# Kernel optimization log

Measured on AMD Instinct MI355X. Metric: run time of the kernel, lower is better.

Reference implementation:

```python
import jax, jax.numpy as jnp
import numpy as np

N = 100000   # num nodes
D = 128      # node_emb_dim
R = 8        # num_relations
E = 1600000  # num edges


def setup_inputs() -> dict:
    key = jax.random.key(0)
    k0, k1, k2, k3, k4 = jax.random.split(key, 5)
    x = jax.random.normal(k0, (N, D), dtype=jnp.float32)
    edge_index = jax.random.randint(k1, (2, E), 0, N, dtype=jnp.int32)
    edge_type = jax.random.randint(k2, (E,), 0, R, dtype=jnp.int32)
    scale = 1.0 / np.sqrt(D)
    W = (jax.random.normal(k3, (R, D, D), dtype=jnp.float32) * scale)       # per-relation weight
    W_root = (jax.random.normal(k4, (D, D), dtype=jnp.float32) * scale)     # root (self-loop) weight
    bias = jnp.zeros((D,), dtype=jnp.float32)
    return {"x": x, "W": W, "W_root": W_root, "bias": bias,
            "edge_index": edge_index, "edge_type": edge_type}


def reference(x, W, W_root, bias, edge_index, edge_type):
    # PyG RGCNConv (num_bases=None, aggr='mean', root_weight=True, bias=True):
    # out_i = x_i @ W_root + bias + sum_r mean_{j in N_r(i)} x_j @ W_r
    # Mean aggregation is linear, so aggregate neighbor features per (node, relation)
    # first, then apply the per-relation transform (avoids [E,D,D] intermediates).
    src, dst = edge_index[0], edge_index[1]
    seg = dst * R + edge_type                                   # [E] segment id per (dst, rel)
    cnt = jax.ops.segment_sum(jnp.ones((E,), x.dtype), seg, num_segments=N * R)  # [N*R]
    sums = jax.ops.segment_sum(x[src], seg, num_segments=N * R)                   # [N*R, D]
    mean = sums / jnp.maximum(cnt, 1.0)[:, None]                                  # [N*R, D]
    rel_out = jnp.einsum('nrd,rde->ne', mean.reshape(N, R, D), W)                 # [N, D]
    return rel_out + x @ W_root + bias
```

## Files before the change

kernel.cpp:

```cpp
#include <hip/hip_runtime.h>


constexpr int D = 128;
constexpr int R = 8;
constexpr int TILE = 2048;
constexpr int CW = 64;
constexpr int LDA = 40;

typedef __bf16 bf16x8 __attribute__((ext_vector_type(8)));
typedef float  f32x4  __attribute__((ext_vector_type(4)));
typedef unsigned short u16x8 __attribute__((ext_vector_type(8)));
typedef unsigned short u16x4 __attribute__((ext_vector_type(4)));

__device__ __forceinline__ unsigned short f2bf(float f) {
    unsigned u = __builtin_bit_cast(unsigned, f);
    u += 0x7FFFu + ((u >> 16) & 1u);
    return (unsigned short)(u >> 16);
}
__device__ __forceinline__ float bf2f(unsigned short h) {
    return __builtin_bit_cast(float, (unsigned)h << 16);
}

constexpr int XB = 768;
constexpr int CB = 512;
__global__ __launch_bounds__(256)
void pre_kernel(const float* __restrict__ x, unsigned short* __restrict__ xbf, int nquad,
                const int* __restrict__ dst, const int* __restrict__ et,
                int* __restrict__ meta, int E) {
    if (blockIdx.x < XB) {
        int stride = XB * 256;
        for (int i = blockIdx.x * 256 + threadIdx.x; i < nquad; i += stride) {
            float4 v = ((const float4*)x)[i];
            u16x4 o;
            o[0] = f2bf(v.x); o[1] = f2bf(v.y); o[2] = f2bf(v.z); o[3] = f2bf(v.w);
            ((u16x4*)xbf)[i] = o;
        }
    } else {
        __shared__ int cnt8[8];
        if (threadIdx.x < 8) cnt8[threadIdx.x] = 0;
        __syncthreads();
        int stride = CB * 256;
        for (int e = (blockIdx.x - XB) * 256 + threadIdx.x; e < E; e += stride) {
            int seg = dst[e] * R + et[e];
            atomicAdd(&cnt8[(seg >> 7) & 7], 1);
        }
        __syncthreads();
        if (threadIdx.x < 8) atomicAdd(&meta[threadIdx.x], cnt8[threadIdx.x]);
    }
}

__global__ void bscan_kernel(int* __restrict__ meta) {
    if (threadIdx.x == 0) {
        int cum = 0;
        for (int p = 0; p < 8; ++p) {
            meta[8 + p]  = cum;
            meta[16 + p] = cum;
            cum += meta[p];
        }
    }
}

__global__ __launch_bounds__(256)
void bucketA_kernel(const int* __restrict__ src, const int* __restrict__ dst,
                    const int* __restrict__ et, int* __restrict__ ebuf_seg,
                    int* __restrict__ ebuf_src, int* __restrict__ meta, int E) {
    __shared__ int cntw[4][8];
    __shared__ int basew[4][8];
    const int tid = threadIdx.x;
    const int w   = tid >> 6;
    for (int t0 = blockIdx.x * TILE; t0 < E; t0 += gridDim.x * TILE) {
        if (tid < 32) cntw[tid >> 3][tid & 7] = 0;
        __syncthreads();
        int seg[8], sr[8], pt[8];
        bool ok[8];
        #pragma unroll
        for (int j = 0; j < 8; ++j) {
            int e = t0 + j * 256 + tid;
            ok[j] = e < E;
            if (ok[j]) {
                seg[j] = dst[e] * R + et[e];
                sr[j]  = src[e];
                pt[j]  = (seg[j] >> 7) & 7;
                atomicAdd(&cntw[w][pt[j]], 1);
            }
        }
        __syncthreads();
        if (tid < 8) {
            int p = tid;
            int tot = cntw[0][p] + cntw[1][p] + cntw[2][p] + cntw[3][p];
            int b = atomicAdd(&meta[16 + p], tot);
            basew[0][p] = b;               b += cntw[0][p];
            basew[1][p] = b;               b += cntw[1][p];
            basew[2][p] = b;               b += cntw[2][p];
            basew[3][p] = b;
            cntw[0][p] = 0; cntw[1][p] = 0; cntw[2][p] = 0; cntw[3][p] = 0;
        }
        __syncthreads();
        #pragma unroll
        for (int j = 0; j < 8; ++j) {
            if (ok[j]) {
                int r   = atomicAdd(&cntw[w][pt[j]], 1);
                int pos = basew[w][pt[j]] + r;
                ebuf_seg[pos] = seg[j];
                ebuf_src[pos] = sr[j];
            }
        }
        __syncthreads();
    }
}

__global__ __launch_bounds__(256)
void hist_kernel(const int* __restrict__ ebuf_seg, const int* __restrict__ meta,
                 int* __restrict__ hist) {
    int part = blockIdx.x & 7;
    int nb   = gridDim.x >> 3;
    int lo   = meta[8 + part];
    int n    = meta[part];
    for (int i = (blockIdx.x >> 3) * 256 + threadIdx.x; i < n; i += nb * 256)
        atomicAdd(&hist[ebuf_seg[lo + i]], 1);
}

__global__ __launch_bounds__(256)
void block_sums_kernel(const int* __restrict__ hs, int* __restrict__ bsum, int n) {
    __shared__ int sh[256];
    int i = blockIdx.x * 256 + threadIdx.x;
    sh[threadIdx.x] = (i < n) ? hs[i] : 0;
    __syncthreads();
    for (int off = 128; off > 0; off >>= 1) {
        if (threadIdx.x < off) sh[threadIdx.x] += sh[threadIdx.x + off];
        __syncthreads();
    }
    if (threadIdx.x == 0) bsum[blockIdx.x] = sh[0];
}

__global__ __launch_bounds__(64)
void scan_bsum_kernel(int* __restrict__ bsum, int nb) {
    int lane = threadIdx.x;
    int carry = 0;
    for (int base = 0; base < nb; base += 64) {
        int i = base + lane;
        int orig = (i < nb) ? bsum[i] : 0;
        int v = orig;
        #pragma unroll
        for (int off = 1; off < 64; off <<= 1) {
            int u = __shfl_up(v, off, 64);
            if (lane >= off) v += u;
        }
        int tot = __shfl(v, 63, 64);
        if (i < nb) bsum[i] = carry + (v - orig);
        carry += tot;
    }
}

__global__ __launch_bounds__(256)
void scan_block_kernel(int* __restrict__ hs, const int* __restrict__ bsum,
                       int* __restrict__ cursor, int n, int E) {
    __shared__ int sh[256];
    int tid = threadIdx.x;
    int i = blockIdx.x * 256 + tid;
    int v = (i < n) ? hs[i] : 0;
    sh[tid] = v;
    __syncthreads();
    for (int off = 1; off < 256; off <<= 1) {
        int u = (tid >= off) ? sh[tid - off] : 0;
        __syncthreads();
        sh[tid] += u;
        __syncthreads();
    }
    int st = bsum[blockIdx.x] + sh[tid] - v;
    if (i < n) { hs[i] = st; cursor[i] = st; }
    if (i == n) hs[n] = E;
}

__global__ __launch_bounds__(256)
void bucketB_kernel(const int* __restrict__ ebuf_seg, const int* __restrict__ ebuf_src,
                    const int* __restrict__ meta, int* __restrict__ cursor,
                    int* __restrict__ spack) {
    int part = blockIdx.x & 7;
    int nb   = gridDim.x >> 3;
    int lo   = meta[8 + part];
    int n    = meta[part];
    for (int i = (blockIdx.x >> 3) * 256 + threadIdx.x; i < n; i += nb * 256) {
        int seg = ebuf_seg[lo + i];
        int s   = ebuf_src[lo + i];
        int pos = atomicAdd(&cursor[seg], 1);
        spack[pos] = s;
    }
}

__global__ __launch_bounds__(256)
void aggregate_kernel(const unsigned short* __restrict__ xbf,
                      const int* __restrict__ spack,
                      const int* __restrict__ hstart,
                      unsigned short* __restrict__ mean,
                      int nseg, int c0) {
    int idx = blockIdx.x * 256 + threadIdx.x;
    int seg = idx >> 3;
    int c8  = idx & 7;
    if (seg >= nseg) return;
    int p0 = hstart[seg], p1 = hstart[seg + 1];
    int coff = c0 + c8 * 8;
    float a[8] = {};
    for (int p = p0; p < p1; p += 4) {
        int s0 = spack[p];
        int s1 = (p + 1 < p1) ? spack[p + 1] : -1;
        int s2 = (p + 2 < p1) ? spack[p + 2] : -1;
        int s3 = (p + 3 < p1) ? spack[p + 3] : -1;
        u16x8 v0 = *(const u16x8*)(xbf + ((size_t)s0 << 7) + coff);
        #pragma unroll
        for (int j = 0; j < 8; ++j) a[j] += bf2f(v0[j]);
        if (s1 >= 0) {
            u16x8 v = *(const u16x8*)(xbf + ((size_t)s1 << 7) + coff);
            #pragma unroll
            for (int j = 0; j < 8; ++j) a[j] += bf2f(v[j]);
        }
        if (s2 >= 0) {
            u16x8 v = *(const u16x8*)(xbf + ((size_t)s2 << 7) + coff);
            #pragma unroll
            for (int j = 0; j < 8; ++j) a[j] += bf2f(v[j]);
        }
        if (s3 >= 0) {
            u16x8 v = *(const u16x8*)(xbf + ((size_t)s3 << 7) + coff);
            #pragma unroll
            for (int j = 0; j < 8; ++j) a[j] += bf2f(v[j]);
        }
    }
    float inv = (p1 > p0) ? 1.0f / (float)(p1 - p0) : 0.0f;
    u16x8 o;
    #pragma unroll
    for (int j = 0; j < 8; ++j) o[j] = f2bf(a[j] * inv);
    *(u16x8*)(mean + ((size_t)seg << 6) + c8 * 8) = o;
}

__global__ __launch_bounds__(256)
void wallt_kernel(const float* __restrict__ Wroot, const float* __restrict__ W,
                  unsigned short* __restrict__ WallTc) {
    int idx = blockIdx.x * 256 + threadIdx.x;
    if (idx >= 128 * 1152) return;
    int n = idx / 1152, k = idx % 1152;
    float v = (k < 1024) ? W[(size_t)(k >> 7) * 16384 + (size_t)(k & 127) * 128 + n]
                         : Wroot[(size_t)(k - 1024) * 128 + n];
    WallTc[idx] = f2bf(v);
}

template<bool FIRST>
__global__ __launch_bounds__(256)
void mfma_gemm_kernel(const unsigned short* __restrict__ xbf,
                      const unsigned short* __restrict__ mean,
                      const unsigned short* __restrict__ WallTc,
                      const float* __restrict__ bias,
                      float* __restrict__ out,
                      int N, int c0) {
    constexpr int NT = FIRST ? 20 : 16;
    __shared__ unsigned short As[64 * LDA];
    __shared__ unsigned short Bs[128 * LDA];
    const int tid  = threadIdx.x;
    const int nd0  = blockIdx.x * 64;
    const int lane = tid & 63;
    const int wid  = tid >> 6;
    const int wm   = wid >> 1;
    const int wn   = wid & 1;
    const int arow = tid >> 2;
    const int aoct = tid & 3;
    const int brow = tid >> 1;
    const int bhalf = tid & 1;

    f32x4 acc[2][4] = {};

    const int  anode = nd0 + arow;
    const bool aok   = anode < N;

    for (int kt = 0; kt < NT; ++kt) {
        if (kt) __syncthreads();
        u16x8 av8;
        #pragma unroll
        for (int j = 0; j < 8; ++j) av8[j] = 0;
        int kbase;
        if (FIRST && kt < 4) {
            if (aok)
                av8 = *(const u16x8*)(xbf + ((size_t)anode << 7) + kt * 32 + aoct * 8);
            kbase = 1024 + kt * 32;
        } else {
            int lk = (kt - (FIRST ? 4 : 0)) * 32;
            if (aok)
                av8 = *(const u16x8*)(mean + ((size_t)anode << 9) + lk + aoct * 8);
            kbase = (lk >> 6) * 128 + c0 + (lk & 63);
        }
        const u16x8* wp = (const u16x8*)(WallTc + (size_t)brow * 1152 + kbase + bhalf * 16);
        u16x8 b0 = wp[0], b1 = wp[1];

        *(u16x8*)&As[arow * LDA + aoct * 8]       = av8;
        *(u16x8*)&Bs[brow * LDA + bhalf * 16]     = b0;
        *(u16x8*)&Bs[brow * LDA + bhalf * 16 + 8] = b1;
        __syncthreads();

        const int ko = (lane >> 4) * 8;
        const int rl = lane & 15;
        bf16x8 af[2], bf[4];
        #pragma unroll
        for (int f = 0; f < 2; ++f)
            af[f] = __builtin_bit_cast(bf16x8,
                *(const u16x8*)&As[(wm * 32 + f * 16 + rl) * LDA + ko]);
        #pragma unroll
        for (int f = 0; f < 4; ++f)
            bf[f] = __builtin_bit_cast(bf16x8,
                *(const u16x8*)&Bs[(wn * 64 + f * 16 + rl) * LDA + ko]);
        #pragma unroll
        for (int mf = 0; mf < 2; ++mf)
            #pragma unroll
            for (int nf = 0; nf < 4; ++nf)
                acc[mf][nf] = __builtin_amdgcn_mfma_f32_16x16x32_bf16(af[mf], bf[nf],
                                                                     acc[mf][nf], 0, 0, 0);
    }

    const int rl = lane & 15;
    const int rg = lane >> 4;
    #pragma unroll
    for (int nf = 0; nf < 4; ++nf) {
        int n = wn * 64 + nf * 16 + rl;
        float bb = FIRST ? bias[n] : 0.0f;
        #pragma unroll
        for (int mf = 0; mf < 2; ++mf) {
            #pragma unroll
            for (int i = 0; i < 4; ++i) {
                int nd = nd0 + wm * 32 + mf * 16 + rg * 4 + i;
                if (nd < N) {
                    size_t o = (size_t)nd * 128 + n;
                    if (FIRST) out[o] = acc[mf][nf][i] + bb;
                    else       out[o] += acc[mf][nf][i];
                }
            }
        }
    }
}

extern "C" void kernel_launch(void* const* d_in, const int* in_sizes, int n_in,
                              void* d_out, int out_size, void* d_ws, size_t ws_size,
                              hipStream_t stream) {
    const float* x     = (const float*)d_in[0];
    const float* W     = (const float*)d_in[1];
    const float* Wroot = (const float*)d_in[2];
    const float* bias  = (const float*)d_in[3];
    const int*   ei    = (const int*)d_in[4];
    const int*   et    = (const int*)d_in[5];
    float*       out   = (float*)d_out;

    const int N = in_sizes[0] / D;
    const int E = in_sizes[5];
    const int* src = ei;
    const int* dst = ei + E;

    const int NSEG = N * R;
    const int NB   = (NSEG + 256) / 256;

    const size_t mean_bytes   = (size_t)NSEG * CW * 2;
    const size_t xbf_bytes    = (size_t)N * D * 2;
    const size_t walltc_bytes = (size_t)128 * 1152 * 2;
    const size_t need = mean_bytes + xbf_bytes + walltc_bytes +
                        ((size_t)(NSEG + 1) + NSEG + E + NB + 32 + 2 * (size_t)E) * 4 + 256;
    if (ws_size < need) return;

    char* p = (char*)d_ws;
    unsigned short* mean   = (unsigned short*)p;  p += mean_bytes;
    unsigned short* xbf    = (unsigned short*)p;  p += xbf_bytes;
    unsigned short* WallTc = (unsigned short*)p;  p += walltc_bytes;
    int* hstart   = (int*)p;  p += (size_t)(NSEG + 1) * 4;
    int* cursor   = (int*)p;  p += (size_t)NSEG * 4;
    int* spack    = (int*)p;  p += (size_t)E * 4;
    int* bsum     = (int*)p;  p += (size_t)NB * 4;
    int* meta     = (int*)p;  p += 32 * 4;
    int* ebuf_seg = (int*)p;  p += (size_t)E * 4;
    int* ebuf_src = (int*)p;

    hipMemsetAsync(hstart, 0, (size_t)(NSEG + 1) * 4, stream);
    hipMemsetAsync(meta, 0, 32 * 4, stream);

    pre_kernel<<<XB + CB, 256, 0, stream>>>(x, xbf, N * D / 4, dst, et, meta, E);
    bscan_kernel<<<1, 64, 0, stream>>>(meta);
    bucketA_kernel<<<(E + TILE - 1) / TILE, 256, 0, stream>>>(
        src, dst, et, ebuf_seg, ebuf_src, meta, E);
    hist_kernel<<<768, 256, 0, stream>>>(ebuf_seg, meta, hstart);
    block_sums_kernel<<<NB, 256, 0, stream>>>(hstart, bsum, NSEG);
    scan_bsum_kernel<<<1, 64, 0, stream>>>(bsum, NB);
    scan_block_kernel<<<NB, 256, 0, stream>>>(hstart, bsum, cursor, NSEG, E);
    bucketB_kernel<<<768, 256, 0, stream>>>(ebuf_seg, ebuf_src, meta, cursor, spack);

    wallt_kernel<<<(128 * 1152 + 255) / 256, 256, 0, stream>>>(Wroot, W, WallTc);

    const int gx = (N + 63) / 64;
    for (int c = 0; c < 2; ++c) {
        int c0 = c * CW;
        aggregate_kernel<<<(NSEG * 8 + 255) / 256, 256, 0, stream>>>(
            xbf, spack, hstart, mean, NSEG, c0);
        if (c == 0)
            mfma_gemm_kernel<true><<<gx, 256, 0, stream>>>(
                xbf, mean, WallTc, bias, out, N, c0);
        else
            mfma_gemm_kernel<false><<<gx, 256, 0, stream>>>(
                xbf, mean, WallTc, bias, out, N, c0);
    }
}
```

Before: 416.7 us.

## Replace two-level segment sort with run-bucketed placement and in-block local sort

Replaces the multi-pass counting sort (partition bucketing, global histogram over all segments, block scans, atomic scatter) with a coarse sort into runs of 128 segments. A per-tile count, column scan and run scan give deterministic placement of packed (src, segment-low-bits) words. The aggregate kernel then sorts each run locally in shared memory by its 7-bit segment id and accumulates per segment. This removes the large per-segment histogram, the cursor atomics and the extra edge buffers. In exchange it adds a serial column scan over tiles, repeats the local sort in both channel passes, and packs the source index into 24 bits, which caps node count.

```diff
diff --git a/kernel.cpp b/kernel.cpp
--- a/kernel.cpp
+++ b/kernel.cpp
@@ -3,9 +3,11 @@
 
 constexpr int D = 128;
 constexpr int R = 8;
-constexpr int TILE = 2048;
 constexpr int CW = 64;
 constexpr int LDA = 40;
+constexpr int TILE2 = 4096;
+constexpr int CAP = 3072;
+constexpr int MAXRUNS = 8192;
 
 typedef __bf16 bf16x8 __attribute__((ext_vector_type(8)));
 typedef float  f32x4  __attribute__((ext_vector_type(4)));
@@ -21,125 +23,59 @@
     return __builtin_bit_cast(float, (unsigned)h << 16);
 }
 
-constexpr int XB = 768;
-constexpr int CB = 512;
-__global__ __launch_bounds__(256)
-void pre_kernel(const float* __restrict__ x, unsigned short* __restrict__ xbf, int nquad,
-                const int* __restrict__ dst, const int* __restrict__ et,
-                int* __restrict__ meta, int E) {
-    if (blockIdx.x < XB) {
-        int stride = XB * 256;
-        for (int i = blockIdx.x * 256 + threadIdx.x; i < nquad; i += stride) {
-            float4 v = ((const float4*)x)[i];
-            u16x4 o;
-            o[0] = f2bf(v.x); o[1] = f2bf(v.y); o[2] = f2bf(v.z); o[3] = f2bf(v.w);
-            ((u16x4*)xbf)[i] = o;
-        }
-    } else {
-        __shared__ int cnt8[8];
-        if (threadIdx.x < 8) cnt8[threadIdx.x] = 0;
-        __syncthreads();
-        int stride = CB * 256;
-        for (int e = (blockIdx.x - XB) * 256 + threadIdx.x; e < E; e += stride) {
+__global__ __launch_bounds__(256)
+void xbf_kernel(const float* __restrict__ x, unsigned short* __restrict__ xbf, int nquad) {
+    int stride = gridDim.x * 256;
+    for (int i = blockIdx.x * 256 + threadIdx.x; i < nquad; i += stride) {
+        float4 v = ((const float4*)x)[i];
+        u16x4 o;
+        o[0] = f2bf(v.x); o[1] = f2bf(v.y); o[2] = f2bf(v.z); o[3] = f2bf(v.w);
+        ((u16x4*)xbf)[i] = o;
+    }
+}
+
+__global__ __launch_bounds__(256)
+void count_kernel(const int* __restrict__ dst, const int* __restrict__ et,
+                  int* __restrict__ counts, int E, int nruns) {
+    __shared__ int lh[MAXRUNS];
+    for (int i = threadIdx.x; i < nruns; i += 256) lh[i] = 0;
+    __syncthreads();
+    int t0 = blockIdx.x * TILE2;
+    #pragma unroll 4
+    for (int j = 0; j < TILE2 / 256; ++j) {
+        int e = t0 + j * 256 + threadIdx.x;
+        if (e < E) {
             int seg = dst[e] * R + et[e];
-            atomicAdd(&cnt8[(seg >> 7) & 7], 1);
-        }
-        __syncthreads();
-        if (threadIdx.x < 8) atomicAdd(&meta[threadIdx.x], cnt8[threadIdx.x]);
-    }
-}
-
-__global__ void bscan_kernel(int* __restrict__ meta) {
-    if (threadIdx.x == 0) {
-        int cum = 0;
-        for (int p = 0; p < 8; ++p) {
-            meta[8 + p]  = cum;
-            meta[16 + p] = cum;
-            cum += meta[p];
-        }
-    }
-}
-
-__global__ __launch_bounds__(256)
-void bucketA_kernel(const int* __restrict__ src, const int* __restrict__ dst,
-                    const int* __restrict__ et, int* __restrict__ ebuf_seg,
-                    int* __restrict__ ebuf_src, int* __restrict__ meta, int E) {
-    __shared__ int cntw[4][8];
-    __shared__ int basew[4][8];
-    const int tid = threadIdx.x;
-    const int w   = tid >> 6;
-    for (int t0 = blockIdx.x * TILE; t0 < E; t0 += gridDim.x * TILE) {
-        if (tid < 32) cntw[tid >> 3][tid & 7] = 0;
-        __syncthreads();
-        int seg[8], sr[8], pt[8];
-        bool ok[8];
-        #pragma unroll
-        for (int j = 0; j < 8; ++j) {
-            int e = t0 + j * 256 + tid;
-            ok[j] = e < E;
-            if (ok[j]) {
-                seg[j] = dst[e] * R + et[e];
-                sr[j]  = src[e];
-                pt[j]  = (seg[j] >> 7) & 7;
-                atomicAdd(&cntw[w][pt[j]], 1);
-            }
-        }
-        __syncthreads();
-        if (tid < 8) {
-            int p = tid;
-            int tot = cntw[0][p] + cntw[1][p] + cntw[2][p] + cntw[3][p];
-            int b = atomicAdd(&meta[16 + p], tot);
-            basew[0][p] = b;               b += cntw[0][p];
-            basew[1][p] = b;               b += cntw[1][p];
-            basew[2][p] = b;               b += cntw[2][p];
-            basew[3][p] = b;
-            cntw[0][p] = 0; cntw[1][p] = 0; cntw[2][p] = 0; cntw[3][p] = 0;
-        }
-        __syncthreads();
-        #pragma unroll
-        for (int j = 0; j < 8; ++j) {
-            if (ok[j]) {
-                int r   = atomicAdd(&cntw[w][pt[j]], 1);
-                int pos = basew[w][pt[j]] + r;
-                ebuf_seg[pos] = seg[j];
-                ebuf_src[pos] = sr[j];
-            }
-        }
-        __syncthreads();
-    }
-}
-
-__global__ __launch_bounds__(256)
-void hist_kernel(const int* __restrict__ ebuf_seg, const int* __restrict__ meta,
-                 int* __restrict__ hist) {
-    int part = blockIdx.x & 7;
-    int nb   = gridDim.x >> 3;
-    int lo   = meta[8 + part];
-    int n    = meta[part];
-    for (int i = (blockIdx.x >> 3) * 256 + threadIdx.x; i < n; i += nb * 256)
-        atomicAdd(&hist[ebuf_seg[lo + i]], 1);
-}
-
-__global__ __launch_bounds__(256)
-void block_sums_kernel(const int* __restrict__ hs, int* __restrict__ bsum, int n) {
-    __shared__ int sh[256];
-    int i = blockIdx.x * 256 + threadIdx.x;
-    sh[threadIdx.x] = (i < n) ? hs[i] : 0;
+            atomicAdd(&lh[seg >> 7], 1);
+        }
+    }
     __syncthreads();
-    for (int off = 128; off > 0; off >>= 1) {
-        if (threadIdx.x < off) sh[threadIdx.x] += sh[threadIdx.x + off];
-        __syncthreads();
-    }
-    if (threadIdx.x == 0) bsum[blockIdx.x] = sh[0];
+    int* row = counts + (size_t)blockIdx.x * nruns;
+    for (int i = threadIdx.x; i < nruns; i += 256) row[i] = lh[i];
+}
+
+__global__ __launch_bounds__(256)
+void colscan_kernel(int* __restrict__ counts, int* __restrict__ runtot,
+                    int ntiles, int nruns) {
+    int r = blockIdx.x * 256 + threadIdx.x;
+    if (r >= nruns) return;
+    int acc = 0;
+    for (int t = 0; t < ntiles; ++t) {
+        size_t idx = (size_t)t * nruns + r;
+        int v = counts[idx];
+        counts[idx] = acc;
+        acc += v;
+    }
+    runtot[r] = acc;
 }
 
 __global__ __launch_bounds__(64)
-void scan_bsum_kernel(int* __restrict__ bsum, int nb) {
+void runscan_kernel(const int* __restrict__ runtot, int* __restrict__ runbase, int nb) {
     int lane = threadIdx.x;
     int carry = 0;
     for (int base = 0; base < nb; base += 64) {
         int i = base + lane;
-        int orig = (i < nb) ? bsum[i] : 0;
+        int orig = (i < nb) ? runtot[i] : 0;
         int v = orig;
         #pragma unroll
         for (int off = 1; off < 64; off <<= 1) {
@@ -147,89 +83,130 @@
             if (lane >= off) v += u;
         }
         int tot = __shfl(v, 63, 64);
-        if (i < nb) bsum[i] = carry + (v - orig);
+        if (i < nb) runbase[i] = carry + (v - orig);
         carry += tot;
     }
-}
-
-__global__ __launch_bounds__(256)
-void scan_block_kernel(int* __restrict__ hs, const int* __restrict__ bsum,
-                       int* __restrict__ cursor, int n, int E) {
-    __shared__ int sh[256];
-    int tid = threadIdx.x;
-    int i = blockIdx.x * 256 + tid;
-    int v = (i < n) ? hs[i] : 0;
-    sh[tid] = v;
+    if (lane == 0) runbase[nb] = carry;
+}
+
+__global__ __launch_bounds__(256)
+void place_kernel(const int* __restrict__ src, const int* __restrict__ dst,
+                  const int* __restrict__ et, const int* __restrict__ counts,
+                  const int* __restrict__ runbase, unsigned* __restrict__ epack,
+                  int E, int nruns) {
+    __shared__ int lh[MAXRUNS];
+    for (int i = threadIdx.x; i < nruns; i += 256) lh[i] = 0;
     __syncthreads();
-    for (int off = 1; off < 256; off <<= 1) {
-        int u = (tid >= off) ? sh[tid - off] : 0;
-        __syncthreads();
-        sh[tid] += u;
-        __syncthreads();
-    }
-    int st = bsum[blockIdx.x] + sh[tid] - v;
-    if (i < n) { hs[i] = st; cursor[i] = st; }
-    if (i == n) hs[n] = E;
-}
-
-__global__ __launch_bounds__(256)
-void bucketB_kernel(const int* __restrict__ ebuf_seg, const int* __restrict__ ebuf_src,
-                    const int* __restrict__ meta, int* __restrict__ cursor,
-                    int* __restrict__ spack) {
-    int part = blockIdx.x & 7;
-    int nb   = gridDim.x >> 3;
-    int lo   = meta[8 + part];
-    int n    = meta[part];
-    for (int i = (blockIdx.x >> 3) * 256 + threadIdx.x; i < n; i += nb * 256) {
-        int seg = ebuf_seg[lo + i];
-        int s   = ebuf_src[lo + i];
-        int pos = atomicAdd(&cursor[seg], 1);
-        spack[pos] = s;
+    int t0 = blockIdx.x * TILE2;
+    const int* colpre = counts + (size_t)blockIdx.x * nruns;
+    #pragma unroll 4
+    for (int j = 0; j < TILE2 / 256; ++j) {
+        int e = t0 + j * 256 + threadIdx.x;
+        if (e < E) {
+            int seg  = dst[e] * R + et[e];
+            int run  = seg >> 7;
+            int rank = atomicAdd(&lh[run], 1);
+            int pos  = runbase[run] + colpre[run] + rank;
+            epack[pos] = (unsigned)src[e] | ((unsigned)(seg & 127) << 24);
+        }
     }
 }
 
 __global__ __launch_bounds__(256)
 void aggregate_kernel(const unsigned short* __restrict__ xbf,
-                      const int* __restrict__ spack,
-                      const int* __restrict__ hstart,
+                      const unsigned* __restrict__ epack,
+                      const int* __restrict__ runbase,
                       unsigned short* __restrict__ mean,
                       int nseg, int c0) {
-    int idx = blockIdx.x * 256 + threadIdx.x;
-    int seg = idx >> 3;
-    int c8  = idx & 7;
-    if (seg >= nseg) return;
-    int p0 = hstart[seg], p1 = hstart[seg + 1];
-    int coff = c0 + c8 * 8;
-    float a[8] = {};
-    for (int p = p0; p < p1; p += 4) {
-        int s0 = spack[p];
-        int s1 = (p + 1 < p1) ? spack[p + 1] : -1;
-        int s2 = (p + 2 < p1) ? spack[p + 2] : -1;
-        int s3 = (p + 3 < p1) ? spack[p + 3] : -1;
-        u16x8 v0 = *(const u16x8*)(xbf + ((size_t)s0 << 7) + coff);
-        #pragma unroll
-        for (int j = 0; j < 8; ++j) a[j] += bf2f(v0[j]);
-        if (s1 >= 0) {
-            u16x8 v = *(const u16x8*)(xbf + ((size_t)s1 << 7) + coff);
+    __shared__ unsigned raw[CAP];
+    __shared__ unsigned srt[CAP];
+    __shared__ int hist[128], sc[128], offs[128], cur[128];
+
+    const int tid  = threadIdx.x;
+    const int run  = blockIdx.x;
+    const int base = runbase[run];
+    const int size = runbase[run + 1] - base;
+    const int c8   = tid & 7;
+    const int sg0  = tid >> 3;
+
+    float a[4][8] = {};
+    int   cacc[4] = {};
+
+    const int nchunks = (size + CAP - 1) / CAP;
+    for (int ch = 0; ch < nchunks; ++ch) {
+        int off = ch * CAP;
+        int n   = min(CAP, size - off);
+
+        if (tid < 128) hist[tid] = 0;
+        __syncthreads();
+        for (int j = tid; j < n; j += 256) {
+            unsigned e = epack[base + off + j];
+            raw[j] = e;
+            atomicAdd(&hist[e >> 24], 1);
+        }
+        __syncthreads();
+        if (tid < 128) sc[tid] = hist[tid];
+        __syncthreads();
+        for (int o = 1; o < 128; o <<= 1) {
+            int u = 0;
+            if (tid < 128 && tid >= o) u = sc[tid - o];
+            __syncthreads();
+            if (tid < 128) sc[tid] += u;
+            __syncthreads();
+        }
+        if (tid < 128) { int x0 = sc[tid] - hist[tid]; offs[tid] = x0; cur[tid] = x0; }
+        __syncthreads();
+        for (int j = tid; j < n; j += 256) {
+            unsigned e = raw[j];
+            int r = atomicAdd(&cur[e >> 24], 1);
+            srt[r] = e;
+        }
+        __syncthreads();
+        #pragma unroll
+        for (int i = 0; i < 4; ++i) {
+            int s  = sg0 + i * 32;
+            int st = offs[s], cn = hist[s];
+            cacc[i] += cn;
+            for (int k = 0; k < cn; k += 4) {
+                unsigned e0 = srt[st + k];
+                int s1ok = (k + 1 < cn), s2ok = (k + 2 < cn), s3ok = (k + 3 < cn);
+                unsigned e1 = s1ok ? srt[st + k + 1] : 0;
+                unsigned e2 = s2ok ? srt[st + k + 2] : 0;
+                unsigned e3 = s3ok ? srt[st + k + 3] : 0;
+                u16x8 v0 = *(const u16x8*)(xbf + ((size_t)(e0 & 0xFFFFFF) << 7) + c0 + c8 * 8);
+                #pragma unroll
+                for (int q = 0; q < 8; ++q) a[i][q] += bf2f(v0[q]);
+                if (s1ok) {
+                    u16x8 v = *(const u16x8*)(xbf + ((size_t)(e1 & 0xFFFFFF) << 7) + c0 + c8 * 8);
+                    #pragma unroll
+                    for (int q = 0; q < 8; ++q) a[i][q] += bf2f(v[q]);
+                }
+                if (s2ok) {
+                    u16x8 v = *(const u16x8*)(xbf + ((size_t)(e2 & 0xFFFFFF) << 7) + c0 + c8 * 8);
+                    #pragma unroll
+                    for (int q = 0; q < 8; ++q) a[i][q] += bf2f(v[q]);
+                }
+                if (s3ok) {
+                    u16x8 v = *(const u16x8*)(xbf + ((size_t)(e3 & 0xFFFFFF) << 7) + c0 + c8 * 8);
+                    #pragma unroll
+                    for (int q = 0; q < 8; ++q) a[i][q] += bf2f(v[q]);
+                }
+            }
+        }
+        __syncthreads();
+    }
+
+    #pragma unroll
+    for (int i = 0; i < 4; ++i) {
+        int seg = run * 128 + sg0 + i * 32;
+        if (seg < nseg) {
+            float inv = (cacc[i] > 0) ? 1.0f / (float)cacc[i] : 0.0f;
+            u16x8 o;
             #pragma unroll
-            for (int j = 0; j < 8; ++j) a[j] += bf2f(v[j]);
-        }
-        if (s2 >= 0) {
-            u16x8 v = *(const u16x8*)(xbf + ((size_t)s2 << 7) + coff);
-            #pragma unroll
-            for (int j = 0; j < 8; ++j) a[j] += bf2f(v[j]);
-        }
-        if (s3 >= 0) {
-            u16x8 v = *(const u16x8*)(xbf + ((size_t)s3 << 7) + coff);
-            #pragma unroll
-            for (int j = 0; j < 8; ++j) a[j] += bf2f(v[j]);
-        }
-    }
-    float inv = (p1 > p0) ? 1.0f / (float)(p1 - p0) : 0.0f;
-    u16x8 o;
-    #pragma unroll
-    for (int j = 0; j < 8; ++j) o[j] = f2bf(a[j] * inv);
-    *(u16x8*)(mean + ((size_t)seg << 6) + c8 * 8) = o;
+            for (int q = 0; q < 8; ++q) o[q] = f2bf(a[i][q] * inv);
+            *(u16x8*)(mean + ((size_t)seg << 6) + c8 * 8) = o;
+        }
+    }
 }
 
 __global__ __launch_bounds__(256)
@@ -350,48 +327,40 @@
     const int* src = ei;
     const int* dst = ei + E;
 
-    const int NSEG = N * R;
-    const int NB   = (NSEG + 256) / 256;
+    const int NSEG   = N * R;
+    const int NRUNS  = (NSEG + 127) / 128;
+    const int NTILES = (E + TILE2 - 1) / TILE2;
+    if (NRUNS > MAXRUNS) return;
 
     const size_t mean_bytes   = (size_t)NSEG * CW * 2;
     const size_t xbf_bytes    = (size_t)N * D * 2;
     const size_t walltc_bytes = (size_t)128 * 1152 * 2;
-    const size_t need = mean_bytes + xbf_bytes + walltc_bytes +
-                        ((size_t)(NSEG + 1) + NSEG + E + NB + 32 + 2 * (size_t)E) * 4 + 256;
+    const size_t counts_bytes = (size_t)NTILES * NRUNS * 4;
+    const size_t need = mean_bytes + xbf_bytes + walltc_bytes + counts_bytes +
+                        ((size_t)NRUNS + (NRUNS + 1) + E) * 4 + 256;
     if (ws_size < need) return;
 
     char* p = (char*)d_ws;
     unsigned short* mean   = (unsigned short*)p;  p += mean_bytes;
     unsigned short* xbf    = (unsigned short*)p;  p += xbf_bytes;
     unsigned short* WallTc = (unsigned short*)p;  p += walltc_bytes;
-    int* hstart   = (int*)p;  p += (size_t)(NSEG + 1) * 4;
-    int* cursor   = (int*)p;  p += (size_t)NSEG * 4;
-    int* spack    = (int*)p;  p += (size_t)E * 4;
-    int* bsum     = (int*)p;  p += (size_t)NB * 4;
-    int* meta     = (int*)p;  p += 32 * 4;
-    int* ebuf_seg = (int*)p;  p += (size_t)E * 4;
-    int* ebuf_src = (int*)p;
-
-    hipMemsetAsync(hstart, 0, (size_t)(NSEG + 1) * 4, stream);
-    hipMemsetAsync(meta, 0, 32 * 4, stream);
-
-    pre_kernel<<<XB + CB, 256, 0, stream>>>(x, xbf, N * D / 4, dst, et, meta, E);
-    bscan_kernel<<<1, 64, 0, stream>>>(meta);
-    bucketA_kernel<<<(E + TILE - 1) / TILE, 256, 0, stream>>>(
-        src, dst, et, ebuf_seg, ebuf_src, meta, E);
-    hist_kernel<<<768, 256, 0, stream>>>(ebuf_seg, meta, hstart);
-    block_sums_kernel<<<NB, 256, 0, stream>>>(hstart, bsum, NSEG);
-    scan_bsum_kernel<<<1, 64, 0, stream>>>(bsum, NB);
-    scan_block_kernel<<<NB, 256, 0, stream>>>(hstart, bsum, cursor, NSEG, E);
-    bucketB_kernel<<<768, 256, 0, stream>>>(ebuf_seg, ebuf_src, meta, cursor, spack);
-
+    int*      counts  = (int*)p;       p += counts_bytes;
+    int*      runtot  = (int*)p;       p += (size_t)NRUNS * 4;
+    int*      runbase = (int*)p;       p += (size_t)(NRUNS + 1) * 4;
+    unsigned* epack   = (unsigned*)p;
+
+    xbf_kernel<<<1024, 256, 0, stream>>>(x, xbf, N * D / 4);
     wallt_kernel<<<(128 * 1152 + 255) / 256, 256, 0, stream>>>(Wroot, W, WallTc);
+
+    count_kernel<<<NTILES, 256, 0, stream>>>(dst, et, counts, E, NRUNS);
+    colscan_kernel<<<(NRUNS + 255) / 256, 256, 0, stream>>>(counts, runtot, NTILES, NRUNS);
+    runscan_kernel<<<1, 64, 0, stream>>>(runtot, runbase, NRUNS);
+    place_kernel<<<NTILES, 256, 0, stream>>>(src, dst, et, counts, runbase, epack, E, NRUNS);
 
     const int gx = (N + 63) / 64;
     for (int c = 0; c < 2; ++c) {
         int c0 = c * CW;
-        aggregate_kernel<<<(NSEG * 8 + 255) / 256, 256, 0, stream>>>(
-            xbf, spack, hstart, mean, NSEG, c0);
+        aggregate_kernel<<<NRUNS, 256, 0, stream>>>(xbf, epack, runbase, mean, NSEG, c0);
         if (c == 0)
             mfma_gemm_kernel<true><<<gx, 256, 0, stream>>>(
                 xbf, mean, WallTc, bias, out, N, c0);
```

Result: slower. 444.8 us (+6.7%).
